# Kernel tuning notes

Measured on AMD Instinct MI355X. Metric: run time of the kernel, lower is better.

Reference implementation:

```python
import jax, jax.numpy as jnp
import numpy as np

N, E, H, EF, NG = 50000, 600000, 128, 4, 20
R_MIN, R_MAX = 0.0, 10.0

def setup_inputs() -> dict:
    key = jax.random.key(0)
    ks = jax.random.split(key, 20)
    s = lambda fi, fo: 1.0 / np.sqrt(fi)
    inp = {
        'h': jax.random.normal(ks[0], (N, H), jnp.float32),
        'x': jax.random.normal(ks[1], (N, 3), jnp.float32),
        'edge_index': jax.random.randint(ks[2], (2, E), 0, N, jnp.int32),
        'mask_ligand': jnp.ones((N,), jnp.float32),
        'edge_attr': jax.random.normal(ks[3], (E, EF), jnp.float32),
        # edge_mlp: Linear(2H+EF+NG,H) silu Linear(H,H) silu
        'We1': jax.random.normal(ks[4], (2*H+EF+NG, H), jnp.float32) * s(2*H+EF+NG, H),
        'be1': jnp.zeros((H,), jnp.float32),
        'We2': jax.random.normal(ks[5], (H, H), jnp.float32) * s(H, H),
        'be2': jnp.zeros((H,), jnp.float32),
        # edge_inf: Linear(H,1) sigmoid
        'Winf': jax.random.normal(ks[6], (H, 1), jnp.float32) * s(H, 1),
        'binf': jnp.zeros((1,), jnp.float32),
        # x_mlp: Linear(H,H) silu Linear(H,1,no bias, gain 0.001) tanh
        'Wx1': jax.random.normal(ks[7], (H, H), jnp.float32) * s(H, H),
        'bx1': jnp.zeros((H,), jnp.float32),
        'Wx2': jax.random.normal(ks[8], (H, 1), jnp.float32) * (0.001 * s(H, 1)),
        # node_mlp: Linear(2H,H) silu Linear(H,H)
        'Wn1': jax.random.normal(ks[9], (2*H, H), jnp.float32) * s(2*H, H),
        'bn1': jnp.zeros((H,), jnp.float32),
        'Wn2': jax.random.normal(ks[10], (H, H), jnp.float32) * s(H, H),
        'bn2': jnp.zeros((H,), jnp.float32),
    }
    return inp

def _gaussian_smearing(d):
    # d: [E,1] -> [E,NG]
    offset = jnp.linspace(R_MIN, R_MAX, NG, dtype=d.dtype)
    coeff = -0.5 / (offset[1] - offset[0]) ** 2
    return jnp.exp(coeff * (d - offset) ** 2)

def reference(h, x, edge_index, mask_ligand, edge_attr,
              We1, be1, We2, be2, Winf, binf, Wx1, bx1, Wx2,
              Wn1, bn1, Wn2, bn2):
    src, dst = edge_index[0], edge_index[1]
    hi, hj = h[dst], h[src]                      # [E,H]
    rel_x = x[dst] - x[src]                      # [E,3]
    d_sq = jnp.sum(rel_x ** 2, -1, keepdims=True)  # [E,1]
    d = jnp.sqrt(d_sq + 1e-8)
    d_feat = _gaussian_smearing(d)               # [E,NG]
    edge_feat = jnp.concatenate([d_feat, edge_attr], -1)
    inp = jnp.concatenate([hi, hj, edge_feat], -1)  # [E,2H+NG+EF]
    mij = jax.nn.silu(jax.nn.silu(inp @ We1 + be1) @ We2 + be2)  # [E,H]
    eij = jax.nn.sigmoid(mij @ Winf + binf)       # [E,1]
    n = h.shape[0]
    mi = jax.ops.segment_sum(mij * eij, dst, num_segments=n)  # [N,H]
    h_new = h + (jax.nn.silu(jnp.concatenate([mi, h], -1) @ Wn1 + bn1) @ Wn2 + bn2)
    gate = jnp.tanh(jax.nn.silu(mij @ Wx1 + bx1) @ Wx2)        # [E,1]
    delta_x = jax.ops.segment_sum(rel_x / (d + 1.0) * gate, dst, num_segments=n)
    x_new = x + delta_x * mask_ligand[:, None]
    return h_new, x_new
```

## Files before the change

### kernel.cpp

```cpp
#include <hip/hip_runtime.h>
#include <hip/hip_bf16.h>
#include <cstdint>

#define NN 50000
#define NE 600000
#define HD 128
#define NG 20
#define EF 4
#define K1 280
#define TILES (NE/64)
#define EGRID 512
#define ROWU 148
#define NTILE 782

typedef __attribute__((ext_vector_type(4))) float f32x4;
typedef __attribute__((ext_vector_type(8))) __bf16 bf16x8;
typedef __attribute__((ext_vector_type(4))) unsigned int u32x4;

__device__ __forceinline__ float fast_rcp(float x){ return __builtin_amdgcn_rcpf(x); }
__device__ __forceinline__ float silu_f(float x){ return x * fast_rcp(1.0f + __expf(-x)); }
__device__ __forceinline__ float sigmoid_f(float x){ return fast_rcp(1.0f + __expf(-x)); }
__device__ __forceinline__ float tanh_f(float x){ return 1.0f - 2.0f*fast_rcp(__expf(2.0f*x)+1.0f); }

__device__ __forceinline__ uint32_t pk2(float a, float b){
  uint32_t ua = __float_as_uint(a); ua += 0x7FFFu + ((ua>>16)&1u);
  uint32_t ub = __float_as_uint(b); ub += 0x7FFFu + ((ub>>16)&1u);
  return (ua>>16) | (ub & 0xFFFF0000u);
}
__device__ __forceinline__ uint16_t bfb(float a){
  uint32_t ua = __float_as_uint(a); ua += 0x7FFFu + ((ua>>16)&1u);
  return (uint16_t)(ua>>16);
}
__device__ __forceinline__ float bf2f(uint16_t b){ return __uint_as_float(((uint32_t)b)<<16); }
__device__ __forceinline__ f32x4 MF(u32x4 a, u32x4 b, f32x4 c){
  return __builtin_amdgcn_mfma_f32_16x16x32_bf16(
      __builtin_bit_cast(bf16x8, a), __builtin_bit_cast(bf16x8, b), c, 0, 0, 0);
}

#define EDGE_LDS_U32 (64*ROWU + 4096 + 4096 + 448)
#define EDGE_LDS_B (EDGE_LDS_U32*4)

__global__ void __launch_bounds__(512, 4) edge_kernel(
    const float* __restrict__ h, const float* __restrict__ x,
    const int* __restrict__ ei, const float* __restrict__ eattr,
    const float* __restrict__ We1, const float* __restrict__ be1,
    const float* __restrict__ We2, const float* __restrict__ be2,
    const float* __restrict__ Winf, const float* __restrict__ binf,
    const float* __restrict__ Wx1, const float* __restrict__ bx1,
    const float* __restrict__ Wx2, float* __restrict__ out)
{
  extern __shared__ uint32_t smem[];
  uint32_t* s_inp = smem;
  uint16_t* t1f   = (uint16_t*)(smem + 64*ROWU);
  uint16_t* mf_   = (uint16_t*)(smem + 64*ROWU + 4096);
  uint32_t* tl    = smem + 64*ROWU + 8192;
  int*   s_dst  = (int*)tl;
  float* s_rel  = (float*)(tl+64);
  float* s_dist = (float*)(tl+256);
  float* s_pe   = (float*)(tl+320);
  float* s_pg   = (float*)(tl+384);

  const int tid = threadIdx.x;
  const int w = tid >> 6, l = tid & 63;
  const int lo = l & 15, hi = l >> 4;
  const int col = w*16 + lo;

  u32x4 B1[9], B2[4], B3[4];
  #pragma unroll
  for (int ks = 0; ks < 9; ++ks){
    float f[8];
    #pragma unroll
    for (int j = 0; j < 8; ++j){
      const int k = ks*32 + hi*8 + j;
      f[j] = (k < K1) ? We1[k*HD + col] : 0.0f;
    }
    B1[ks] = {pk2(f[0],f[1]), pk2(f[2],f[3]), pk2(f[4],f[5]), pk2(f[6],f[7])};
  }
  #pragma unroll
  for (int ks = 0; ks < 4; ++ks){
    float f2[8], f3[8];
    #pragma unroll
    for (int j = 0; j < 8; ++j){
      const int k = ks*32 + hi*8 + j;
      f2[j] = We2[k*HD + col];
      f3[j] = Wx1[k*HD + col];
    }
    B2[ks] = {pk2(f2[0],f2[1]), pk2(f2[2],f2[3]), pk2(f2[4],f2[5]), pk2(f2[6],f2[7])};
    B3[ks] = {pk2(f3[0],f3[1]), pk2(f3[2],f3[3]), pk2(f3[4],f3[5]), pk2(f3[6],f3[7])};
  }
  const float vbe1 = be1[col], vbe2 = be2[col], vbx1 = bx1[col];
  const float wi = Winf[col], wx = Wx2[col], vbinf = binf[0];
  const float SP = 10.0f/19.0f;
  const float CO = -0.5f/(SP*SP);
  const int r8 = tid >> 3, p8 = tid & 7;
  const int ks2 = w >> 1;
  const int lp  = ((w&1)*2 + (lo>>3))*16 + 4*hi;
  const int jj  = lo & 7;

  for (int t = blockIdx.x; t < TILES; t += EGRID){
    const int ebase = t*64;
    __syncthreads();

    if (tid < 64){
      const int e = ebase + tid;
      const int sj = ei[e], dj = ei[NE + e];
      s_dst[tid] = dj;
      const float ax = x[dj*3+0]-x[sj*3+0];
      const float ay = x[dj*3+1]-x[sj*3+1];
      const float az = x[dj*3+2]-x[sj*3+2];
      const float dd = sqrtf(ax*ax + ay*ay + az*az + 1e-8f);
      s_rel[3*tid+0]=ax; s_rel[3*tid+1]=ay; s_rel[3*tid+2]=az;
      s_dist[tid]=dd; s_pe[tid]=0.0f; s_pg[tid]=0.0f;
      float g[32];
      #pragma unroll
      for (int j = 0; j < 20; ++j){ const float a = dd - j*SP; g[j] = __expf(CO*a*a); }
      const float4 e4 = *reinterpret_cast<const float4*>(eattr + (size_t)e*EF);
      g[20]=e4.x; g[21]=e4.y; g[22]=e4.z; g[23]=e4.w;
      #pragma unroll
      for (int j = 24; j < 32; ++j) g[j] = 0.0f;
      #pragma unroll
      for (int q = 0; q < 16; ++q) s_inp[tid*ROWU + 128 + q] = pk2(g[2*q], g[2*q+1]);
    }
    {
      const int e = ebase + r8;
      const int node = (p8 < 4) ? ei[NE + e] : ei[e];
      const float* hp = h + (size_t)node*HD + (p8 & 3)*32;
      uint32_t* dp = s_inp + r8*ROWU + p8*16;
      #pragma unroll
      for (int q = 0; q < 8; ++q){
        const float4 v = *reinterpret_cast<const float4*>(hp + 4*q);
        dp[2*q]   = pk2(v.x, v.y);
        dp[2*q+1] = pk2(v.z, v.w);
      }
    }
    __syncthreads();

    #pragma unroll
    for (int Mt = 0; Mt < 4; ++Mt){
      const uint32_t* arow = s_inp + (Mt*16 + lo)*ROWU + hi*4;
      f32x4 acc = {0,0,0,0};
      #pragma unroll
      for (int ks = 0; ks < 9; ++ks){
        const u32x4 A = *reinterpret_cast<const u32x4*>(arow + ks*16);
        acc = MF(A, B1[ks], acc);
      }
      uint16_t* tp = t1f + ((Mt*4 + ks2)*64 + lp)*8 + jj;
      #pragma unroll
      for (int reg = 0; reg < 4; ++reg)
        tp[reg*8] = bfb(silu_f(acc[reg] + vbe1));
    }
    __syncthreads();

    #pragma unroll
    for (int Mt = 0; Mt < 4; ++Mt){
      f32x4 acc = {0,0,0,0};
      #pragma unroll
      for (int ks = 0; ks < 4; ++ks){
        const u32x4 A = *reinterpret_cast<const u32x4*>(t1f + ((Mt*4+ks)*64 + l)*8);
        acc = MF(A, B2[ks], acc);
      }
      uint16_t* mp = mf_ + ((Mt*4 + ks2)*64 + lp)*8 + jj;
      float p[4];
      #pragma unroll
      for (int reg = 0; reg < 4; ++reg){
        const float m = silu_f(acc[reg] + vbe2);
        mp[reg*8] = bfb(m);
        p[reg] = m * wi;
      }
      #pragma unroll
      for (int msk = 1; msk < 16; msk <<= 1){
        #pragma unroll
        for (int reg = 0; reg < 4; ++reg) p[reg] += __shfl_xor(p[reg], msk);
      }
      if (lo == 0){
        #pragma unroll
        for (int reg = 0; reg < 4; ++reg) atomicAdd(&s_pe[Mt*16 + 4*hi + reg], p[reg]);
      }
    }
    __syncthreads();

    #pragma unroll
    for (int Mt = 0; Mt < 4; ++Mt){
      #pragma unroll
      for (int reg = 0; reg < 4; ++reg){
        const int r = Mt*16 + 4*hi + reg;
        const float eij = sigmoid_f(s_pe[r] + vbinf);
        const float m = bf2f(mf_[((Mt*4 + ks2)*64 + lp + reg)*8 + jj]);
        atomicAdd(out + (size_t)s_dst[r]*HD + col, m*eij);
      }
    }
    #pragma unroll
    for (int Mt = 0; Mt < 4; ++Mt){
      f32x4 acc = {0,0,0,0};
      #pragma unroll
      for (int ks = 0; ks < 4; ++ks){
        const u32x4 A = *reinterpret_cast<const u32x4*>(mf_ + ((Mt*4+ks)*64 + l)*8);
        acc = MF(A, B3[ks], acc);
      }
      float p[4];
      #pragma unroll
      for (int reg = 0; reg < 4; ++reg)
        p[reg] = silu_f(acc[reg] + vbx1) * wx;
      #pragma unroll
      for (int msk = 1; msk < 16; msk <<= 1){
        #pragma unroll
        for (int reg = 0; reg < 4; ++reg) p[reg] += __shfl_xor(p[reg], msk);
      }
      if (lo == 0){
        #pragma unroll
        for (int reg = 0; reg < 4; ++reg) atomicAdd(&s_pg[Mt*16 + 4*hi + reg], p[reg]);
      }
    }
    __syncthreads();

    if (tid < 192){
      const int er = tid/3, c = tid - 3*er;
      const float gate = tanh_f(s_pg[er]);
      const float sc = gate * fast_rcp(s_dist[er] + 1.0f);
      atomicAdd(out + (size_t)NN*HD + (size_t)s_dst[er]*3 + c, s_rel[3*er+c]*sc);
    }
  }
}

#define CROW 132

__global__ void __launch_bounds__(512, 4) node_kernel(
    const float* __restrict__ h, const float* __restrict__ x,
    const float* __restrict__ mask,
    const float* __restrict__ Wn1, const float* __restrict__ bn1,
    const float* __restrict__ Wn2, const float* __restrict__ bn2,
    float* __restrict__ out)
{
  __shared__ uint32_t s_cat[64*CROW];
  __shared__ __align__(16) uint16_t t1n[4*4*64*8];

  const int tid = threadIdx.x;
  const int w = tid >> 6, l = tid & 63;
  const int lo = l & 15, hi = l >> 4;
  const int col = w*16 + lo;

  u32x4 Bn1[8], Bn2[4];
  #pragma unroll
  for (int ks = 0; ks < 8; ++ks){
    float f[8];
    #pragma unroll
    for (int j = 0; j < 8; ++j) f[j] = Wn1[(ks*32 + hi*8 + j)*HD + col];
    Bn1[ks] = {pk2(f[0],f[1]), pk2(f[2],f[3]), pk2(f[4],f[5]), pk2(f[6],f[7])};
  }
  #pragma unroll
  for (int ks = 0; ks < 4; ++ks){
    float f[8];
    #pragma unroll
    for (int j = 0; j < 8; ++j) f[j] = Wn2[(ks*32 + hi*8 + j)*HD + col];
    Bn2[ks] = {pk2(f[0],f[1]), pk2(f[2],f[3]), pk2(f[4],f[5]), pk2(f[6],f[7])};
  }
  const float vbn1 = bn1[col], vbn2 = bn2[col];
  const int nbase = blockIdx.x*64;
  const int ks2 = w >> 1;
  const int lp  = ((w&1)*2 + (lo>>3))*16 + 4*hi;
  const int jj  = lo & 7;

  {
    const int r = tid >> 3, p = tid & 7;
    const int n = nbase + r;
    uint32_t* dp = s_cat + r*CROW + p*16;
    if (n < NN){
      const float* sp = (p < 4) ? (out + (size_t)n*HD + p*32)
                                : (h   + (size_t)n*HD + (p-4)*32);
      #pragma unroll
      for (int q = 0; q < 8; ++q){
        const float4 v = *reinterpret_cast<const float4*>(sp + 4*q);
        dp[2*q]   = pk2(v.x, v.y);
        dp[2*q+1] = pk2(v.z, v.w);
      }
    } else {
      #pragma unroll
      for (int q = 0; q < 16; ++q) dp[q] = 0u;
    }
  }
  __syncthreads();

  #pragma unroll
  for (int Mt = 0; Mt < 4; ++Mt){
    const uint32_t* arow = s_cat + (Mt*16 + lo)*CROW + hi*4;
    f32x4 acc = {0,0,0,0};
    #pragma unroll
    for (int ks = 0; ks < 8; ++ks){
      const u32x4 A = *reinterpret_cast<const u32x4*>(arow + ks*16);
      acc = MF(A, Bn1[ks], acc);
    }
    uint16_t* tp = t1n + ((Mt*4 + ks2)*64 + lp)*8 + jj;
    #pragma unroll
    for (int reg = 0; reg < 4; ++reg)
      tp[reg*8] = bfb(silu_f(acc[reg] + vbn1));
  }
  __syncthreads();

  #pragma unroll
  for (int Mt = 0; Mt < 4; ++Mt){
    f32x4 acc = {0,0,0,0};
    #pragma unroll
    for (int ks = 0; ks < 4; ++ks){
      const u32x4 A = *reinterpret_cast<const u32x4*>(t1n + ((Mt*4+ks)*64 + l)*8);
      acc = MF(A, Bn2[ks], acc);
    }
    #pragma unroll
    for (int reg = 0; reg < 4; ++reg){
      const int n = nbase + Mt*16 + 4*hi + reg;
      if (n < NN)
        out[(size_t)n*HD + col] = h[(size_t)n*HD + col] + acc[reg] + vbn2;
    }
  }

  if (tid < 192){
    const int r = tid/3, c = tid - 3*r;
    const int n = nbase + r;
    if (n < NN){
      const size_t ix = (size_t)NN*HD + (size_t)n*3 + c;
      out[ix] = x[(size_t)n*3 + c] + out[ix]*mask[n];
    }
  }
}

extern "C" void kernel_launch(void* const* d_in, const int* in_sizes, int n_in,
                              void* d_out, int out_size, void* d_ws, size_t ws_size,
                              hipStream_t stream) {
  (void)in_sizes; (void)n_in; (void)d_ws; (void)ws_size;
  const float* h    = (const float*)d_in[0];
  const float* x    = (const float*)d_in[1];
  const int*   ei   = (const int*)  d_in[2];
  const float* mask = (const float*)d_in[3];
  const float* ea   = (const float*)d_in[4];
  const float* We1  = (const float*)d_in[5];
  const float* be1  = (const float*)d_in[6];
  const float* We2  = (const float*)d_in[7];
  const float* be2  = (const float*)d_in[8];
  const float* Winf = (const float*)d_in[9];
  const float* binf = (const float*)d_in[10];
  const float* Wx1  = (const float*)d_in[11];
  const float* bx1  = (const float*)d_in[12];
  const float* Wx2  = (const float*)d_in[13];
  const float* Wn1  = (const float*)d_in[14];
  const float* bn1  = (const float*)d_in[15];
  const float* Wn2  = (const float*)d_in[16];
  const float* bn2  = (const float*)d_in[17];
  float* out = (float*)d_out;

  hipFuncSetAttribute(reinterpret_cast<const void*>(edge_kernel),
                      hipFuncAttributeMaxDynamicSharedMemorySize, EDGE_LDS_B);

  hipMemsetAsync(d_out, 0, (size_t)out_size * sizeof(float), stream);

  edge_kernel<<<EGRID, 512, EDGE_LDS_B, stream>>>(
      h, x, ei, ea, We1, be1, We2, be2, Winf, binf, Wx1, bx1, Wx2, out);
  node_kernel<<<NTILE, 512, 0, stream>>>(
      h, x, mask, Wn1, bn1, Wn2, bn2, out);
}
```

Measured before the change: 465.1 us.

## Prefetch next edge tile into registers and swizzle LDS intermediate layout

The edge kernel now software-pipelines its gathers. Edge indices, h rows, node coordinates and edge attributes for the next tile are loaded into registers while the current tile's first MFMA stage runs, which hides global gather latency behind compute. It also applies an XOR swizzle to the row index of the t1f/mf_ LDS buffers to reduce bank conflicts, and replaces scalar LDS stores with 128-bit vector stores. The cost is higher register pressure from holding 32 floats of prefetched h per thread, which may reduce occupancy.

```diff
diff --git a/kernel.cpp b/kernel.cpp
--- a/kernel.cpp
+++ b/kernel.cpp
@@ -12,6 +12,7 @@
 #define EGRID 512
 #define ROWU 148
 #define NTILE 782
+#define SW(r) ((r) ^ (((r)>>3)&7))
 
 typedef __attribute__((ext_vector_type(4))) float f32x4;
 typedef __attribute__((ext_vector_type(8))) __bf16 bf16x8;
@@ -64,6 +65,11 @@
   const int w = tid >> 6, l = tid & 63;
   const int lo = l & 15, hi = l >> 4;
   const int col = w*16 + lo;
+  const int r8 = tid >> 3, p8 = tid & 7;
+  const int ks2 = w >> 1;
+  const int lp  = ((w&1)*2 + (lo>>3))*16 + 4*hi;
+  const int jj  = lo & 7;
+  const int lsw = SW(l);
 
   u32x4 B1[9], B2[4], B3[4];
   #pragma unroll
@@ -92,62 +98,90 @@
   const float wi = Winf[col], wx = Wx2[col], vbinf = binf[0];
   const float SP = 10.0f/19.0f;
   const float CO = -0.5f/(SP*SP);
-  const int r8 = tid >> 3, p8 = tid & 7;
-  const int ks2 = w >> 1;
-  const int lp  = ((w&1)*2 + (lo>>3))*16 + 4*hi;
-  const int jj  = lo & 7;
+
+  float4 hv[8];
+  int nnode = 0, nsj = 0, ndj = 0;
+  float nxd0=0,nxd1=0,nxd2=0,nxs0=0,nxs1=0,nxs2=0;
+  float4 nea = {0,0,0,0};
+
+  {
+    const int ebase = blockIdx.x*64;
+    const int e = ebase + r8;
+    nnode = (p8 < 4) ? ei[NE+e] : ei[e];
+    if (tid < 64){ nsj = ei[ebase+tid]; ndj = ei[NE+ebase+tid]; }
+    const float* hp = h + (size_t)nnode*HD + (p8&3)*32;
+    #pragma unroll
+    for (int q = 0; q < 8; ++q) hv[q] = *reinterpret_cast<const float4*>(hp + 4*q);
+    if (tid < 64){
+      nxd0 = x[ndj*3+0]; nxd1 = x[ndj*3+1]; nxd2 = x[ndj*3+2];
+      nxs0 = x[nsj*3+0]; nxs1 = x[nsj*3+1]; nxs2 = x[nsj*3+2];
+      nea = *reinterpret_cast<const float4*>(eattr + (size_t)(ebase+tid)*EF);
+    }
+  }
 
   for (int t = blockIdx.x; t < TILES; t += EGRID){
-    const int ebase = t*64;
-    __syncthreads();
-
+    const bool more = (t + EGRID) < TILES;
+    __syncthreads();
+
+    {
+      uint32_t* dp = s_inp + r8*ROWU + p8*16;
+      #pragma unroll
+      for (int q = 0; q < 4; ++q){
+        u32x4 v = { pk2(hv[2*q].x, hv[2*q].y),   pk2(hv[2*q].z, hv[2*q].w),
+                    pk2(hv[2*q+1].x, hv[2*q+1].y), pk2(hv[2*q+1].z, hv[2*q+1].w) };
+        *reinterpret_cast<u32x4*>(dp + 4*q) = v;
+      }
+    }
     if (tid < 64){
-      const int e = ebase + tid;
-      const int sj = ei[e], dj = ei[NE + e];
-      s_dst[tid] = dj;
-      const float ax = x[dj*3+0]-x[sj*3+0];
-      const float ay = x[dj*3+1]-x[sj*3+1];
-      const float az = x[dj*3+2]-x[sj*3+2];
+      const float ax = nxd0-nxs0, ay = nxd1-nxs1, az = nxd2-nxs2;
       const float dd = sqrtf(ax*ax + ay*ay + az*az + 1e-8f);
+      s_dst[tid] = ndj;
       s_rel[3*tid+0]=ax; s_rel[3*tid+1]=ay; s_rel[3*tid+2]=az;
       s_dist[tid]=dd; s_pe[tid]=0.0f; s_pg[tid]=0.0f;
-      float g[32];
+      float g[24];
       #pragma unroll
       for (int j = 0; j < 20; ++j){ const float a = dd - j*SP; g[j] = __expf(CO*a*a); }
-      const float4 e4 = *reinterpret_cast<const float4*>(eattr + (size_t)e*EF);
-      g[20]=e4.x; g[21]=e4.y; g[22]=e4.z; g[23]=e4.w;
-      #pragma unroll
-      for (int j = 24; j < 32; ++j) g[j] = 0.0f;
-      #pragma unroll
-      for (int q = 0; q < 16; ++q) s_inp[tid*ROWU + 128 + q] = pk2(g[2*q], g[2*q+1]);
-    }
-    {
-      const int e = ebase + r8;
-      const int node = (p8 < 4) ? ei[NE + e] : ei[e];
-      const float* hp = h + (size_t)node*HD + (p8 & 3)*32;
-      uint32_t* dp = s_inp + r8*ROWU + p8*16;
-      #pragma unroll
-      for (int q = 0; q < 8; ++q){
-        const float4 v = *reinterpret_cast<const float4*>(hp + 4*q);
-        dp[2*q]   = pk2(v.x, v.y);
-        dp[2*q+1] = pk2(v.z, v.w);
-      }
-    }
-    __syncthreads();
+      g[20]=nea.x; g[21]=nea.y; g[22]=nea.z; g[23]=nea.w;
+      uint32_t* gp = s_inp + tid*ROWU + 128;
+      u32x4 g0 = {pk2(g[0],g[1]),  pk2(g[2],g[3]),  pk2(g[4],g[5]),  pk2(g[6],g[7])};
+      u32x4 g1 = {pk2(g[8],g[9]),  pk2(g[10],g[11]),pk2(g[12],g[13]),pk2(g[14],g[15])};
+      u32x4 g2 = {pk2(g[16],g[17]),pk2(g[18],g[19]),pk2(g[20],g[21]),pk2(g[22],g[23])};
+      u32x4 g3 = {0,0,0,0};
+      *reinterpret_cast<u32x4*>(gp)    = g0;
+      *reinterpret_cast<u32x4*>(gp+4)  = g1;
+      *reinterpret_cast<u32x4*>(gp+8)  = g2;
+      *reinterpret_cast<u32x4*>(gp+12) = g3;
+    }
+    __syncthreads();
+
+    const int nbase = (t + EGRID)*64;
+    if (more){
+      const int e = nbase + r8;
+      nnode = (p8 < 4) ? ei[NE+e] : ei[e];
+      if (tid < 64){ nsj = ei[nbase+tid]; ndj = ei[NE+nbase+tid]; }
+    }
 
     #pragma unroll
     for (int Mt = 0; Mt < 4; ++Mt){
       const uint32_t* arow = s_inp + (Mt*16 + lo)*ROWU + hi*4;
       f32x4 acc = {0,0,0,0};
       #pragma unroll
-      for (int ks = 0; ks < 9; ++ks){
-        const u32x4 A = *reinterpret_cast<const u32x4*>(arow + ks*16);
-        acc = MF(A, B1[ks], acc);
-      }
-      uint16_t* tp = t1f + ((Mt*4 + ks2)*64 + lp)*8 + jj;
+      for (int ks = 0; ks < 9; ++ks)
+        acc = MF(*reinterpret_cast<const u32x4*>(arow + ks*16), B1[ks], acc);
       #pragma unroll
       for (int reg = 0; reg < 4; ++reg)
-        tp[reg*8] = bfb(silu_f(acc[reg] + vbe1));
+        t1f[((Mt*4 + ks2)*64 + SW(lp+reg))*8 + jj] = bfb(silu_f(acc[reg] + vbe1));
+    }
+
+    if (more){
+      const float* hp = h + (size_t)nnode*HD + (p8&3)*32;
+      #pragma unroll
+      for (int q = 0; q < 8; ++q) hv[q] = *reinterpret_cast<const float4*>(hp + 4*q);
+      if (tid < 64){
+        nxd0 = x[ndj*3+0]; nxd1 = x[ndj*3+1]; nxd2 = x[ndj*3+2];
+        nxs0 = x[nsj*3+0]; nxs1 = x[nsj*3+1]; nxs2 = x[nsj*3+2];
+        nea = *reinterpret_cast<const float4*>(eattr + (size_t)(nbase+tid)*EF);
+      }
     }
     __syncthreads();
 
@@ -155,16 +189,13 @@
     for (int Mt = 0; Mt < 4; ++Mt){
       f32x4 acc = {0,0,0,0};
       #pragma unroll
-      for (int ks = 0; ks < 4; ++ks){
-        const u32x4 A = *reinterpret_cast<const u32x4*>(t1f + ((Mt*4+ks)*64 + l)*8);
-        acc = MF(A, B2[ks], acc);
-      }
-      uint16_t* mp = mf_ + ((Mt*4 + ks2)*64 + lp)*8 + jj;
+      for (int ks = 0; ks < 4; ++ks)
+        acc = MF(*reinterpret_cast<const u32x4*>(t1f + ((Mt*4+ks)*64 + lsw)*8), B2[ks], acc);
       float p[4];
       #pragma unroll
       for (int reg = 0; reg < 4; ++reg){
         const float m = silu_f(acc[reg] + vbe2);
-        mp[reg*8] = bfb(m);
+        mf_[((Mt*4 + ks2)*64 + SW(lp+reg))*8 + jj] = bfb(m);
         p[reg] = m * wi;
       }
       #pragma unroll
@@ -185,7 +216,7 @@
       for (int reg = 0; reg < 4; ++reg){
         const int r = Mt*16 + 4*hi + reg;
         const float eij = sigmoid_f(s_pe[r] + vbinf);
-        const float m = bf2f(mf_[((Mt*4 + ks2)*64 + lp + reg)*8 + jj]);
+        const float m = bf2f(mf_[((Mt*4 + ks2)*64 + SW(lp+reg))*8 + jj]);
         atomicAdd(out + (size_t)s_dst[r]*HD + col, m*eij);
       }
     }
@@ -193,10 +224,8 @@
     for (int Mt = 0; Mt < 4; ++Mt){
       f32x4 acc = {0,0,0,0};
       #pragma unroll
-      for (int ks = 0; ks < 4; ++ks){
-        const u32x4 A = *reinterpret_cast<const u32x4*>(mf_ + ((Mt*4+ks)*64 + l)*8);
-        acc = MF(A, B3[ks], acc);
-      }
+      for (int ks = 0; ks < 4; ++ks)
+        acc = MF(*reinterpret_cast<const u32x4*>(mf_ + ((Mt*4+ks)*64 + lsw)*8), B3[ks], acc);
       float p[4];
       #pragma unroll
       for (int reg = 0; reg < 4; ++reg)
@@ -285,10 +314,8 @@
     const uint32_t* arow = s_cat + (Mt*16 + lo)*CROW + hi*4;
     f32x4 acc = {0,0,0,0};
     #pragma unroll
-    for (int ks = 0; ks < 8; ++ks){
-      const u32x4 A = *reinterpret_cast<const u32x4*>(arow + ks*16);
-      acc = MF(A, Bn1[ks], acc);
-    }
+    for (int ks = 0; ks < 8; ++ks)
+      acc = MF(*reinterpret_cast<const u32x4*>(arow + ks*16), Bn1[ks], acc);
     uint16_t* tp = t1n + ((Mt*4 + ks2)*64 + lp)*8 + jj;
     #pragma unroll
     for (int reg = 0; reg < 4; ++reg)
@@ -300,10 +327,8 @@
   for (int Mt = 0; Mt < 4; ++Mt){
     f32x4 acc = {0,0,0,0};
     #pragma unroll
-    for (int ks = 0; ks < 4; ++ks){
-      const u32x4 A = *reinterpret_cast<const u32x4*>(t1n + ((Mt*4+ks)*64 + l)*8);
-      acc = MF(A, Bn2[ks], acc);
-    }
+    for (int ks = 0; ks < 4; ++ks)
+      acc = MF(*reinterpret_cast<const u32x4*>(t1n + ((Mt*4+ks)*64 + l)*8), Bn2[ks], acc);
     #pragma unroll
     for (int reg = 0; reg < 4; ++reg){
       const int n = nbase + Mt*16 + 4*hi + reg;
```

Result: slower. 723.6 us (+55.6%).
